# Kernel tuning notes

Measured on AMD Instinct MI355X. Metric: run time of the kernel, lower is better.

Reference implementation:

```python
import jax, jax.numpy as jnp
import numpy as np

B, C, H, W = 64, 192, 56, 56
NH, WS, SS = 6, 7, 3
HD = C // NH
N = WS * WS
MLP_H = int(C * 2.0)
EPS = 1e-5


def _layer_norm(x, g, b):
    m = jnp.mean(x, axis=-1, keepdims=True)
    v = jnp.mean(jnp.square(x - m), axis=-1, keepdims=True)
    return (x - m) * jax.lax.rsqrt(v + EPS) * g + b


def _window_partition(x):  # (B,H,W,C) -> (B*nW, N, C)
    b, h, w, c = x.shape
    x = x.reshape(b, h // WS, WS, w // WS, WS, c)
    return x.transpose(0, 1, 3, 2, 4, 5).reshape(-1, N, c)


def _window_reverse(win, h, w):  # (B*nW, N, C) -> (B,H,W,C)
    b = win.shape[0] // ((h // WS) * (w // WS))
    x = win.reshape(b, h // WS, w // WS, WS, WS, -1)
    return x.transpose(0, 1, 3, 2, 4, 5).reshape(b, h, w, -1)


def setup_inputs() -> dict:
    key = jax.random.key(0)
    ks = jax.random.split(key, 12)
    s = 0.02
    inp = {
        'query': jax.random.normal(ks[0], (B, C, H, W), jnp.float32),
        'norm_q_g': jnp.ones((C,), jnp.float32), 'norm_q_b': jnp.zeros((C,), jnp.float32),
        'norm_kv_g': jnp.ones((C,), jnp.float32), 'norm_kv_b': jnp.zeros((C,), jnp.float32),
        'Wq': jax.random.normal(ks[1], (C, C), jnp.float32) * s, 'bq': jnp.zeros((C,), jnp.float32),
        'Wk': jax.random.normal(ks[2], (C, C), jnp.float32) * s, 'bk': jnp.zeros((C,), jnp.float32),
        'Wv': jax.random.normal(ks[3], (C, C), jnp.float32) * s, 'bv': jnp.zeros((C,), jnp.float32),
        'rpb_table': jax.random.normal(ks[4], ((2 * WS - 1) ** 2, NH), jnp.float32) * s,
        'Wproj': jax.random.normal(ks[5], (C, C), jnp.float32) * s, 'bproj': jnp.zeros((C,), jnp.float32),
        'norm_ffn_g': jnp.ones((C,), jnp.float32), 'norm_ffn_b': jnp.zeros((C,), jnp.float32),
        'W1': jax.random.normal(ks[6], (C, MLP_H), jnp.float32) * s, 'b1': jnp.zeros((MLP_H,), jnp.float32),
        'W2': jax.random.normal(ks[7], (MLP_H, C), jnp.float32) * s, 'b2': jnp.zeros((C,), jnp.float32),
    }
    # relative position index (constant buffer)
    coords = np.stack(np.meshgrid(np.arange(WS), np.arange(WS), indexing='ij')).reshape(2, -1)
    rel = (coords[:, :, None] - coords[:, None, :]).transpose(1, 2, 0)
    rel[..., 0] += WS - 1
    rel[..., 1] += WS - 1
    rel[..., 0] *= 2 * WS - 1
    inp['rel_idx'] = jnp.asarray(rel.sum(-1), jnp.int32)  # (N, N)
    # shifted-window attention mask (constant buffer)
    img = np.zeros((H, W), np.float32)
    cnt = 0
    for hs in (slice(0, -WS), slice(-WS, -SS), slice(-SS, None)):
        for ws_ in (slice(0, -WS), slice(-WS, -SS), slice(-SS, None)):
            img[hs, ws_] = cnt
            cnt += 1
    mw = img.reshape(H // WS, WS, W // WS, WS).transpose(0, 2, 1, 3).reshape(-1, N)
    am = mw[:, None, :] - mw[:, :, None]  # (nW, N, N)
    inp['attn_mask'] = jnp.asarray(np.where(am != 0, -100.0, 0.0), np.float32)
    return inp


def reference(query, norm_q_g, norm_q_b, norm_kv_g, norm_kv_b, Wq, bq, Wk, bk, Wv, bv,
              rpb_table, Wproj, bproj, norm_ffn_g, norm_ffn_b, W1, b1, W2, b2,
              rel_idx, attn_mask):
    scale = HD ** (-0.5)
    x = query.reshape(B, C, H * W).transpose(0, 2, 1)  # (B, HW, C)
    shortcut = x
    qn = _layer_norm(x, norm_q_g, norm_q_b).reshape(B, H, W, C)
    kvn = _layer_norm(x, norm_kv_g, norm_kv_b).reshape(B, H, W, C)
    # cyclic shift
    qn = jnp.roll(qn, (-SS, -SS), axis=(1, 2))
    kvn = jnp.roll(kvn, (-SS, -SS), axis=(1, 2))
    q_win = _window_partition(qn)   # (B_, N, C)
    kv_win = _window_partition(kvn)
    B_ = q_win.shape[0]
    q = (q_win @ Wq + bq).reshape(B_, N, NH, HD).transpose(0, 2, 1, 3)
    k = (kv_win @ Wk + bk).reshape(B_, N, NH, HD).transpose(0, 2, 1, 3)
    v = (kv_win @ Wv + bv).reshape(B_, N, NH, HD).transpose(0, 2, 1, 3)
    attn = jnp.einsum('bhnd,bhmd->bhnm', q * scale, k)  # (B_, NH, N, N)
    bias = rpb_table[rel_idx.reshape(-1)].reshape(N, N, NH).transpose(2, 0, 1)
    attn = attn + bias[None]
    nW = attn_mask.shape[0]
    attn = attn.reshape(B_ // nW, nW, NH, N, N) + attn_mask[None, :, None]
    attn = attn.reshape(B_, NH, N, N)
    attn = jax.nn.softmax(attn, axis=-1)
    out = jnp.einsum('bhnm,bhmd->bhnd', attn, v).transpose(0, 2, 1, 3).reshape(B_, N, C)
    out = out @ Wproj + bproj
    x_sp = _window_reverse(out, H, W)
    x_sp = jnp.roll(x_sp, (SS, SS), axis=(1, 2))  # reverse shift
    x = shortcut + x_sp.reshape(B, H * W, C)
    h = _layer_norm(x, norm_ffn_g, norm_ffn_b)
    h = jax.nn.gelu(h @ W1 + b1, approximate=False) @ W2 + b2
    x = x + h
    return x.transpose(0, 2, 1).reshape(B, C, H, W)
```

## Files before the change

kernel.cpp:

```cpp
#include <hip/hip_runtime.h>
#include <hip/hip_bf16.h>
#include <math.h>

#define B_IMG 64
#define C_DIM 192
#define HW 3136
#define NTOK (B_IMG*HW)
#define NH 6
#define HD 32
#define WSZ 7
#define NTW 49
#define SS 3
#define NWIN 4096
#define NW64 262144
#define MLPH 384
#define EPS 1e-5f

typedef __attribute__((ext_vector_type(8))) short bfx8;
typedef __attribute__((ext_vector_type(4))) float f32x4;

__device__ __forceinline__ float u2f(unsigned short u){
    union { float f; unsigned int i; } v; v.i = ((unsigned int)u) << 16; return v.f;
}
__device__ __forceinline__ unsigned short f2u(float f){
    union { float f; unsigned int i; } v; v.f = f;
    unsigned int r = v.i + 0x7FFF + ((v.i >> 16) & 1);
    return (unsigned short)(r >> 16);
}
__device__ __forceinline__ unsigned int cvtpk(float lo, float hi){
    unsigned int r;
    asm("v_cvt_pk_bf16_f32 %0, %1, %2" : "=v"(r) : "v"(lo), "v"(hi));
    return r;
}
__device__ __forceinline__ void gl_lds16(const void* g, void* l){
    __builtin_amdgcn_global_load_lds(
        (const __attribute__((address_space(1))) unsigned int*)g,
        (__attribute__((address_space(3))) unsigned int*)l, 16, 0, 0);
}

__device__ __forceinline__ int rowmap(int w_, int n){
    int b  = w_ >> 6, wl = w_ & 63;
    int wy = wl >> 3, wx = wl & 7;
    int ty = n / 7,  tx = n % 7;
    int h = wy*7 + ty + SS; if (h >= 56) h -= 56;
    int w = wx*7 + tx + SS; if (w >= 56) w -= 56;
    return b*HW + h*56 + w;
}

__global__ void __launch_bounds__(256) p0_prep(
    const float* Wq, const float* bq, const float* Wk, const float* bk,
    const float* Wv, const float* bv, const float* Wproj,
    const float* W1, const float* b1, const float* W2,
    const float* gq, const float* nbq, const float* gkv, const float* nbkv,
    const float* gffn, const float* nbffn,
    const float* rpb, const int* rel_idx, const float* attn_mask,
    unsigned short* WqkvT, unsigned short* WprojT, unsigned short* W1T, unsigned short* W2T,
    float* bias_qkv, float* b1_e, unsigned short* comb,
    float* colsum_qkv, float* colsum1)
{
    const float scale = 0.17677669529663687f;
    int id = blockIdx.x*256 + threadIdx.x;
    if (id < 110592){
        int j = id/192, c = id - j*192;
        int which = j/192, col = j - which*192;
        float v;
        if (which==0)      v = scale*gq[c]*Wq[c*192+col];
        else if (which==1) v = gkv[c]*Wk[c*192+col];
        else               v = gkv[c]*Wv[c*192+col];
        WqkvT[id] = f2u(v);
    } else if (id < 147456){
        int t = id-110592; int co = t/192, k = t-co*192;
        WprojT[t] = f2u(Wproj[k*192+co]);
    } else if (id < 221184){
        int t = id-147456; int j = t/192, c = t-j*192;
        W1T[t] = f2u(gffn[c]*W1[c*384+j]);
    } else if (id < 294912){
        int t = id-221184; int co = t/384, k = t-co*384;
        W2T[t] = f2u(W2[k*192+co]);
    } else if (id < 295488){
        int j = id-294912; int which=j/192, col=j-which*192;
        float s;
        if (which==0){ s = bq[col]; for(int c=0;c<192;c++) s += nbq[c]*Wq[c*192+col]; s*=scale; }
        else if (which==1){ s = bk[col]; for(int c=0;c<192;c++) s += nbkv[c]*Wk[c*192+col]; }
        else { s = bv[col]; for(int c=0;c<192;c++) s += nbkv[c]*Wv[c*192+col]; }
        bias_qkv[j] = s;
    } else if (id < 295872){
        int j = id-295488; float s = b1[j];
        for(int c=0;c<192;c++) s += nbffn[c]*W1[c*384+j];
        b1_e[j] = s;
    } else if (id < 394176){
        int t = id-295872;
        int j = t & 63, i = (t>>6) & 63;
        int rest = t >> 12;
        int h = rest % 6, cls = rest / 6;
        float v = -1e30f;
        if (i < 49 && j < 49){
            int wlrep = (cls>>1)*56 + (cls&1)*7;
            v = rpb[rel_idx[i*49+j]*6 + h] + attn_mask[wlrep*2401 + i*49 + j];
        }
        comb[t] = f2u(v);
    } else if (id < 394752){
        int j = id-394176; int which=j/192, col=j-which*192;
        float s = 0.f;
        if (which==0){ for(int c=0;c<192;c++) s += gq[c]*Wq[c*192+col]; s*=scale; }
        else if (which==1){ for(int c=0;c<192;c++) s += gkv[c]*Wk[c*192+col]; }
        else { for(int c=0;c<192;c++) s += gkv[c]*Wv[c*192+col]; }
        colsum_qkv[j] = s;
    } else if (id < 395136){
        int j = id-394752; float s = 0.f;
        for(int c=0;c<192;c++) s += gffn[c]*W1[c*384+j];
        colsum1[j] = s;
    }
}

__global__ void __launch_bounds__(256) p1_transpose_stats(
    const float* q, unsigned short* X, float* mean, float* rstd)
{
    __shared__ float t[32*193];
    __shared__ float ms[32], rs[32];
    int blk = blockIdx.x;
    int b = blk / 98, tile = blk - b*98;
    int hw0 = tile*32;
    const float* qb = q + (size_t)b*C_DIM*HW;
    int hw_off = threadIdx.x & 31, csub = threadIdx.x >> 5;
    for (int cb = 0; cb < 192; cb += 8){
        int c = cb + csub;
        t[hw_off*193 + c] = qb[(size_t)c*HW + hw0 + hw_off];
    }
    __syncthreads();
    {
        int tt = threadIdx.x >> 3, qq = threadIdx.x & 7;
        float s=0.f, s2=0.f;
        #pragma unroll
        for (int i=0;i<24;i++){ float v = t[tt*193 + qq*24 + i]; s+=v; s2+=v*v; }
        s  += __shfl_xor(s,1);  s  += __shfl_xor(s,2);  s  += __shfl_xor(s,4);
        s2 += __shfl_xor(s2,1); s2 += __shfl_xor(s2,2); s2 += __shfl_xor(s2,4);
        if (qq==0){
            float m = s*(1.f/192.f);
            ms[tt] = m; rs[tt] = rsqrtf(s2*(1.f/192.f) - m*m + EPS);
        }
    }
    __syncthreads();
    int g0 = b*HW + hw0;
    if (threadIdx.x < 32){
        mean[g0+threadIdx.x] = ms[threadIdx.x];
        rstd[g0+threadIdx.x] = rs[threadIdx.x];
    }
    for (int i = threadIdx.x; i < 32*24; i += 256){
        int tt = i/24, cq = i - tt*24;
        int base = tt*193 + cq*8;
        int4 vr; unsigned int* pu = (unsigned int*)&vr;
        pu[0] = cvtpk(t[base+0], t[base+1]);
        pu[1] = cvtpk(t[base+2], t[base+3]);
        pu[2] = cvtpk(t[base+4], t[base+5]);
        pu[3] = cvtpk(t[base+6], t[base+7]);
        *(int4*)(X + (size_t)(g0+tt)*192 + cq*8) = vr;
    }
}

__global__ void __launch_bounds__(256) p2_qkv(
    const unsigned short* X, const float* mean, const float* rstd,
    const unsigned short* WqkvT, const float* bias_qkv, const float* colsum_qkv,
    unsigned short* Qb, unsigned short* Kb, unsigned short* Vt)
{
    __shared__ __align__(16) char L[32768];
    __shared__ int rowg[64];
    __shared__ __align__(16) float mr[64], rr[64];
    char* As = L; char* Bs = L + 8192;
    int which = blockIdx.y, bx = blockIdx.x;
    if (which < 2 && bx >= 3136) return;
    int t0 = bx*64;
    int tid = threadIdx.x, l = tid&63, wid = tid>>6;
    if (tid < 64){
        int w, n;
        if (which == 2){ w = bx; n = tid > 48 ? 48 : tid; }
        else { int t = t0 + tid; w = t/49; n = t - w*49; }
        int g = rowmap(w, n); rowg[tid]=g; mr[tid]=mean[g]; rr[tid]=rstd[g];
    }
    __syncthreads();
    f32x4 acc[4][3] = {};
    for (int kt=0; kt<3; ++kt){
        #pragma unroll
        for (int i=0;i<2;++i){
            int c = i*256 + tid;
            int row = c>>3, kq = (c&7) ^ (row&7);
            gl_lds16(X + (size_t)rowg[row]*192 + kt*64 + kq*8,
                     As + i*4096 + wid*1024);
        }
        #pragma unroll
        for (int i=0;i<6;++i){
            int c = i*256 + tid;
            int row = c>>3, kq = (c&7) ^ (row&7);
            gl_lds16(WqkvT + (size_t)(which*192+row)*192 + kt*64 + kq*8,
                     Bs + i*4096 + wid*1024);
        }
        __syncthreads();
        #pragma unroll
        for (int ks2=0; ks2<2; ++ks2){
            int kb = ks2*64 + ((l>>4)*16);
            bfx8 a[4], b[3];
            #pragma unroll
            for (int m=0;m<4;m++){ int r = m*16 + (l&15); a[m] = *(const bfx8*)(As + r*128 + (kb ^ ((r&7)<<4))); }
            #pragma unroll
            for (int n=0;n<3;n++){ int r = (wid*3+n)*16 + (l&15); b[n] = *(const bfx8*)(Bs + r*128 + (kb ^ ((r&7)<<4))); }
            #pragma unroll
            for (int m=0;m<4;m++)
                #pragma unroll
                for (int n=0;n<3;n++)
                    acc[m][n] = __builtin_amdgcn_mfma_f32_16x16x32_bf16(a[m], b[n], acc[m][n], 0,0,0);
        }
        __syncthreads();
    }
    unsigned short* Cs = (unsigned short*)L;
    #pragma unroll
    for (int m=0;m<4;m++){
        f32x4 m4 = *(const f32x4*)(mr + m*16 + (l>>4)*4);
        f32x4 r4 = *(const f32x4*)(rr + m*16 + (l>>4)*4);
        #pragma unroll
        for (int n=0;n<3;n++){
            int col = (wid*3+n)*16 + (l&15);
            float bv = bias_qkv[which*192 + col];
            float cs = colsum_qkv[which*192 + col];
            float v0 = r4[0]*(acc[m][n][0] - m4[0]*cs) + bv;
            float v1 = r4[1]*(acc[m][n][1] - m4[1]*cs) + bv;
            float v2 = r4[2]*(acc[m][n][2] - m4[2]*cs) + bv;
            float v3 = r4[3]*(acc[m][n][3] - m4[3]*cs) + bv;
            unsigned int p0 = cvtpk(v0,v1), p1 = cvtpk(v2,v3);
            int row = m*16 + (l>>4)*4;
            Cs[row*200 + col]     = (unsigned short)p0;
            Cs[(row+1)*200 + col] = (unsigned short)(p0>>16);
            Cs[(row+2)*200 + col] = (unsigned short)p1;
            Cs[(row+3)*200 + col] = (unsigned short)(p1>>16);
        }
    }
    __syncthreads();
    if (which < 2){
        unsigned short* dst = which==0 ? Qb : Kb;
        for (int c = tid; c < 64*24; c += 256){
            int row = c/24, cq = c-row*24;
            int4 v = *(const int4*)(Cs + row*200 + cq*8);
            *(int4*)(dst + (size_t)(t0+row)*192 + cq*8) = v;
        }
    } else {
        int w = bx;
        #pragma unroll
        for (int k=0;k<6;++k){
            int c = k*32 + (tid&31); int jo = tid>>5;
            int4 ov; unsigned short* os = (unsigned short*)&ov;
            #pragma unroll
            for (int e=0;e<8;++e) os[e] = Cs[(jo*8+e)*200 + c];
            *(int4*)(Vt + (size_t)c*NW64 + w*64 + jo*8) = ov;
        }
    }
}

__global__ void __launch_bounds__(128) p3_attn(
    const unsigned short* Qb, const unsigned short* Kb, const unsigned short* Vt,
    const unsigned short* comb, unsigned short* attn_h)
{
    __shared__ __align__(16) char PL[2][8448];
    int bid = blockIdx.x;
    int w = bid/3, yp = bid - w*3;
    int tid = threadIdx.x, l = tid & 63;
    int h = yp*2 + (tid>>6);
    char* P = PL[tid>>6];
    float* invr = (float*)(PL[tid>>6] + 8192);
    int q = l & 15, g = l >> 4;
    int wl = w & 63;
    int cls = (((wl>>3)==7) ? 2 : 0) + (((wl&7)==7) ? 1 : 0);

    bfx8 ak[4], bq[4];
    #pragma unroll
    for (int jt=0; jt<4; ++jt){
        int row = 16*jt + q; if (row > 48) row = 48;
        size_t base = (size_t)(w*49 + row)*192 + h*32 + g*8;
        ak[jt] = *(const bfx8*)(Kb + base);
        bq[jt] = *(const bfx8*)(Qb + base);
    }
    f32x4 s[4][4];
    {
        f32x4 z = {0.f,0.f,0.f,0.f};
        #pragma unroll
        for (int it=0; it<4; ++it)
            #pragma unroll
            for (int jt=0; jt<4; ++jt)
                s[it][jt] = __builtin_amdgcn_mfma_f32_16x16x32_bf16(ak[jt], bq[it], z, 0,0,0);
    }
    const unsigned short* cb = comb + ((size_t)(cls*6 + h) << 12);
    float sum[4];
    #pragma unroll
    for (int it=0; it<4; ++it){
        #pragma unroll
        for (int jt=0; jt<4; ++jt){
            uint2 c2 = *(const uint2*)(cb + (16*it + q)*64 + 16*jt + 4*g);
            const unsigned short* cs = (const unsigned short*)&c2;
            s[it][jt][0] += u2f(cs[0]);
            s[it][jt][1] += u2f(cs[1]);
            s[it][jt][2] += u2f(cs[2]);
            s[it][jt][3] += u2f(cs[3]);
        }
        float m = s[it][0][0];
        #pragma unroll
        for (int jt=0; jt<4; ++jt)
            #pragma unroll
            for (int r=0; r<4; ++r) m = fmaxf(m, s[it][jt][r]);
        m = fmaxf(m, __shfl_xor(m, 16));
        m = fmaxf(m, __shfl_xor(m, 32));
        float su = 0.f;
        #pragma unroll
        for (int jt=0; jt<4; ++jt)
            #pragma unroll
            for (int r=0; r<4; ++r){
                float e = __expf(s[it][jt][r] - m);
                s[it][jt][r] = e;
                su += e;
            }
        su += __shfl_xor(su, 16);
        su += __shfl_xor(su, 32);
        sum[it] = su;
    }
    #pragma unroll
    for (int it=0; it<4; ++it){
        int i = 16*it + q;
        #pragma unroll
        for (int jt=0; jt<4; ++jt){
            unsigned int w0 = cvtpk(s[it][jt][0], s[it][jt][1]);
            unsigned int w1 = cvtpk(s[it][jt][2], s[it][jt][3]);
            int jb = 32*jt + 8*g;
            *(uint2*)(P + i*128 + (jb ^ ((i&7)<<4))) = make_uint2(w0, w1);
        }
    }
    if (l < 16){
        #pragma unroll
        for (int it=0; it<4; ++it) invr[16*it + l] = 1.0f / sum[it];
    }
    __syncthreads();
    f32x4 o[4][2] = {};
    #pragma unroll
    for (int kt=0; kt<2; ++kt){
        bfx8 pa[4], vb[2];
        #pragma unroll
        for (int mt=0; mt<4; ++mt){
            int r = 16*mt + q;
            pa[mt] = *(const bfx8*)(P + r*128 + ((kt*64 + g*16) ^ ((r&7)<<4)));
        }
        #pragma unroll
        for (int nt=0; nt<2; ++nt){
            int d = 16*nt + q;
            vb[nt] = *(const bfx8*)(Vt + (size_t)(h*32 + d)*NW64 + w*64 + kt*32 + g*8);
        }
        #pragma unroll
        for (int mt=0; mt<4; ++mt)
            #pragma unroll
            for (int nt=0; nt<2; ++nt)
                o[mt][nt] = __builtin_amdgcn_mfma_f32_16x16x32_bf16(pa[mt], vb[nt], o[mt][nt], 0,0,0);
    }
    #pragma unroll
    for (int mt=0; mt<4; ++mt){
        f32x4 iv = *(const f32x4*)(invr + 16*mt + 4*g);
        #pragma unroll
        for (int nt=0; nt<2; ++nt){
            int d = 16*nt + q;
            #pragma unroll
            for (int r=0; r<4; ++r){
                int i = 16*mt + 4*g + r;
                if (i < 49)
                    attn_h[((size_t)h*NTOK + (size_t)w*49 + i)*32 + d] = f2u(o[mt][nt][r] * iv[r]);
            }
        }
    }
}

__global__ void __launch_bounds__(256) p4_proj(
    const unsigned short* attn_h, const unsigned short* WprojT, const float* bproj,
    const unsigned short* X, unsigned short* x2, float* mean2, float* rstd2)
{
    __shared__ __align__(16) char L[32768];
    __shared__ int rowg[64];
    char* As = L; char* Bs = L + 8192;
    int t0 = blockIdx.x*64;
    int tid = threadIdx.x, l = tid&63, wid = tid>>6;
    if (tid < 64){
        int t = t0 + tid; int w = t/49, n = t - w*49;
        rowg[tid] = rowmap(w, n);
    }
    __syncthreads();
    f32x4 acc[4][3] = {};
    for (int kt=0; kt<3; ++kt){
        #pragma unroll
        for (int i=0;i<2;++i){
            int c = i*256 + tid;
            int row = c>>3, kq = (c&7) ^ (row&7);
            int hh = kt*2 + (kq>>2), kin = kq&3;
            gl_lds16(attn_h + ((size_t)hh*NTOK + t0+row)*32 + kin*8,
                     As + i*4096 + wid*1024);
        }
        #pragma unroll
        for (int i=0;i<6;++i){
            int c = i*256 + tid;
            int row = c>>3, kq = (c&7) ^ (row&7);
            gl_lds16(WprojT + (size_t)row*192 + kt*64 + kq*8,
                     Bs + i*4096 + wid*1024);
        }
        __syncthreads();
        #pragma unroll
        for (int ks2=0; ks2<2; ++ks2){
            int kb = ks2*64 + ((l>>4)*16);
            bfx8 a[4], b[3];
            #pragma unroll
            for (int m=0;m<4;m++){ int r = m*16 + (l&15); a[m] = *(const bfx8*)(As + r*128 + (kb ^ ((r&7)<<4))); }
            #pragma unroll
            for (int n=0;n<3;n++){ int r = (wid*3+n)*16 + (l&15); b[n] = *(const bfx8*)(Bs + r*128 + (kb ^ ((r&7)<<4))); }
            #pragma unroll
            for (int m=0;m<4;m++)
                #pragma unroll
                for (int n=0;n<3;n++)
                    acc[m][n] = __builtin_amdgcn_mfma_f32_16x16x32_bf16(a[m], b[n], acc[m][n], 0,0,0);
        }
        __syncthreads();
    }
    unsigned short* bounce = (unsigned short*)L;
    #pragma unroll
    for (int m=0;m<4;m++)
        #pragma unroll
        for (int n=0;n<3;n++){
            int col = (wid*3+n)*16 + (l&15);
            float bv = bproj[col];
            #pragma unroll
            for (int r=0;r<4;r++){
                int row = m*16 + (l>>4)*4 + r;
                int g = rowg[row];
                bounce[row*200 + col] = f2u(acc[m][n][r] + bv + u2f(X[(size_t)g*192 + col]));
            }
        }
    __syncthreads();
    {
        int row = tid>>2, q = tid&3;
        float s=0.f, s2=0.f;
        #pragma unroll
        for (int i=0;i<6;i++){
            int4 v = *(const int4*)(bounce + row*200 + q*48 + i*8);
            const unsigned short* vs=(const unsigned short*)&v;
            #pragma unroll
            for(int e=0;e<8;e++){ float f=u2f(vs[e]); s+=f; s2+=f*f; }
        }
        s  += __shfl_xor(s,1);  s  += __shfl_xor(s,2);
        s2 += __shfl_xor(s2,1); s2 += __shfl_xor(s2,2);
        if (q==0){
            float m = s*(1.f/192.f);
            mean2[rowg[row]] = m;
            rstd2[rowg[row]] = rsqrtf(s2*(1.f/192.f) - m*m + EPS);
        }
    }
    for (int c = tid; c < 64*24; c += 256){
        int row = c/24, cq = c-row*24;
        int4 v = *(const int4*)(bounce + row*200 + cq*8);
        *(int4*)(x2 + (size_t)rowg[row]*192 + cq*8) = v;
    }
}

__global__ void __launch_bounds__(256) p5_mlp1(
    const unsigned short* x2, const float* mean2, const float* rstd2,
    const unsigned short* W1T, const float* b1_e, const float* colsum1,
    unsigned short* hidden)
{
    __shared__ __align__(16) char L[32768];
    __shared__ __align__(16) float mr[64], rr[64];
    char* As = L; char* Bs = L + 8192;
    int t0 = blockIdx.x*64; int nh = blockIdx.y;
    int tid = threadIdx.x, l = tid&63, wid = tid>>6;
    if (tid < 64){ mr[tid]=mean2[t0+tid]; rr[tid]=rstd2[t0+tid]; }
    __syncthreads();
    f32x4 acc[4][3] = {};
    for (int kt=0; kt<3; ++kt){
        #pragma unroll
        for (int i=0;i<2;++i){
            int c = i*256 + tid;
            int row = c>>3, kq = (c&7) ^ (row&7);
            gl_lds16(x2 + (size_t)(t0+row)*192 + kt*64 + kq*8,
                     As + i*4096 + wid*1024);
        }
        #pragma unroll
        for (int i=0;i<6;++i){
            int c = i*256 + tid;
            int row = c>>3, kq = (c&7) ^ (row&7);
            gl_lds16(W1T + (size_t)(nh*192+row)*192 + kt*64 + kq*8,
                     Bs + i*4096 + wid*1024);
        }
        __syncthreads();
        #pragma unroll
        for (int ks2=0; ks2<2; ++ks2){
            int kb = ks2*64 + ((l>>4)*16);
            bfx8 a[4], b[3];
            #pragma unroll
            for (int m=0;m<4;m++){ int r = m*16 + (l&15); a[m] = *(const bfx8*)(As + r*128 + (kb ^ ((r&7)<<4))); }
            #pragma unroll
            for (int n=0;n<3;n++){ int r = (wid*3+n)*16 + (l&15); b[n] = *(const bfx8*)(Bs + r*128 + (kb ^ ((r&7)<<4))); }
            #pragma unroll
            for (int m=0;m<4;m++)
                #pragma unroll
                for (int n=0;n<3;n++)
                    acc[m][n] = __builtin_amdgcn_mfma_f32_16x16x32_bf16(a[m], b[n], acc[m][n], 0,0,0);
        }
        __syncthreads();
    }
    unsigned short* bounce = (unsigned short*)L;
    #pragma unroll
    for (int m=0;m<4;m++){
        f32x4 m4 = *(const f32x4*)(mr + m*16 + (l>>4)*4);
        f32x4 r4 = *(const f32x4*)(rr + m*16 + (l>>4)*4);
        #pragma unroll
        for (int n=0;n<3;n++){
            int col = (wid*3+n)*16 + (l&15);
            float bv = b1_e[nh*192 + col];
            float cs = colsum1[nh*192 + col];
            float gv[4];
            #pragma unroll
            for (int r=0;r<4;r++){
                float v = r4[r]*(acc[m][n][r] - m4[r]*cs) + bv;
                gv[r] = 0.5f*v*(1.0f + erff(v*0.70710678118654752f));
            }
            unsigned int p0 = cvtpk(gv[0],gv[1]), p1 = cvtpk(gv[2],gv[3]);
            int row = m*16 + (l>>4)*4;
            bounce[row*200 + col]     = (unsigned short)p0;
            bounce[(row+1)*200 + col] = (unsigned short)(p0>>16);
            bounce[(row+2)*200 + col] = (unsigned short)p1;
            bounce[(row+3)*200 + col] = (unsigned short)(p1>>16);
        }
    }
    __syncthreads();
    for (int c = tid; c < 64*24; c += 256){
        int row = c/24, cq = c-row*24;
        int4 v = *(const int4*)(bounce + row*200 + cq*8);
        *(int4*)(hidden + (size_t)(t0+row)*384 + nh*192 + cq*8) = v;
    }
}

__global__ void __launch_bounds__(256) p6_mlp2(
    const unsigned short* hidden, const unsigned short* W2T, const float* b2,
    const unsigned short* x2, float* out)
{
    __shared__ __align__(16) char L[32768];
    char* As = L; char* Bs = L + 8192;
    int t0 = blockIdx.x*64;
    int tid = threadIdx.x, l = tid&63, wid = tid>>6;
    f32x4 acc[4][3] = {};
    for (int kt=0; kt<6; ++kt){
        #pragma unroll
        for (int i=0;i<2;++i){
            int c = i*256 + tid;
            int row = c>>3, kq = (c&7) ^ (row&7);
            gl_lds16(hidden + (size_t)(t0+row)*384 + kt*64 + kq*8,
                     As + i*4096 + wid*1024);
        }
        #pragma unroll
        for (int i=0;i<6;++i){
            int c = i*256 + tid;
            int row = c>>3, kq = (c&7) ^ (row&7);
            gl_lds16(W2T + (size_t)row*384 + kt*64 + kq*8,
                     Bs + i*4096 + wid*1024);
        }
        __syncthreads();
        #pragma unroll
        for (int ks2=0; ks2<2; ++ks2){
            int kb = ks2*64 + ((l>>4)*16);
            bfx8 a[4], b[3];
            #pragma unroll
            for (int m=0;m<4;m++){ int r = m*16 + (l&15); a[m] = *(const bfx8*)(As + r*128 + (kb ^ ((r&7)<<4))); }
            #pragma unroll
            for (int n=0;n<3;n++){ int r = (wid*3+n)*16 + (l&15); b[n] = *(const bfx8*)(Bs + r*128 + (kb ^ ((r&7)<<4))); }
            #pragma unroll
            for (int m=0;m<4;m++)
                #pragma unroll
                for (int n=0;n<3;n++)
                    acc[m][n] = __builtin_amdgcn_mfma_f32_16x16x32_bf16(a[m], b[n], acc[m][n], 0,0,0);
        }
        __syncthreads();
    }
    float* bounce = (float*)L;
    int bimg = t0 / HW, hw0 = t0 - bimg*HW;
    #pragma unroll
    for (int half=0; half<2; ++half){
        #pragma unroll
        for (int mm=0;mm<2;mm++){
            int m = half*2 + mm;
            #pragma unroll
            for (int n=0;n<3;n++){
                int col = (wid*3+n)*16 + (l&15);
                float bv = b2[col];
                #pragma unroll
                for (int r=0;r<4;r++){
                    int row = m*16 + (l>>4)*4 + r;
                    bounce[(row - half*32)*197 + col] = acc[m][n][r] + bv + u2f(x2[(size_t)(t0+row)*192 + col]);
                }
            }
        }
        __syncthreads();
        int hw0h = hw0 + half*32;
        for (int i = tid; i < 32*192; i += 256){
            int cc = i>>5, hwoff = i&31;
            out[(size_t)(bimg*192 + cc)*HW + hw0h + hwoff] = bounce[hwoff*197 + cc];
        }
        __syncthreads();
    }
}

extern "C" void kernel_launch(void* const* d_in, const int* in_sizes, int n_in,
                              void* d_out, int out_size, void* d_ws, size_t ws_size,
                              hipStream_t stream) {
    const float* query = (const float*)d_in[0];
    const float* gq    = (const float*)d_in[1];
    const float* nbq   = (const float*)d_in[2];
    const float* gkv   = (const float*)d_in[3];
    const float* nbkv  = (const float*)d_in[4];
    const float* Wq    = (const float*)d_in[5];
    const float* bq    = (const float*)d_in[6];
    const float* Wk    = (const float*)d_in[7];
    const float* bk    = (const float*)d_in[8];
    const float* Wv    = (const float*)d_in[9];
    const float* bv    = (const float*)d_in[10];
    const float* rpb   = (const float*)d_in[11];
    const float* Wproj = (const float*)d_in[12];
    const float* bproj = (const float*)d_in[13];
    const float* gffn  = (const float*)d_in[14];
    const float* nbffn = (const float*)d_in[15];
    const float* W1    = (const float*)d_in[16];
    const float* b1    = (const float*)d_in[17];
    const float* W2    = (const float*)d_in[18];
    const float* b2    = (const float*)d_in[19];
    const int*   rel_idx   = (const int*)d_in[20];
    const float* attn_mask = (const float*)d_in[21];
    float* out = (float*)d_out;

    char* wsb = (char*)d_ws;
    size_t off = 0;
    auto alloc = [&](size_t bytes)->void*{
        void* p = wsb + off; off += (bytes + 255) & ~(size_t)255; return p;
    };
    unsigned short* X      = (unsigned short*)alloc((size_t)NTOK*192*2);
    unsigned short* Qb     = (unsigned short*)alloc((size_t)NTOK*192*2);
    unsigned short* Kb     = (unsigned short*)alloc((size_t)NTOK*192*2);
    unsigned short* Vt     = (unsigned short*)alloc((size_t)192*NW64*2);
    unsigned short* attn_h = (unsigned short*)alloc((size_t)NH*NTOK*32*2);
    float* mean  = (float*)alloc((size_t)NTOK*4);
    float* rstd  = (float*)alloc((size_t)NTOK*4);
    unsigned short* WqkvT = (unsigned short*)alloc(110592*2);
    unsigned short* WprojT= (unsigned short*)alloc(36864*2);
    unsigned short* W1T   = (unsigned short*)alloc(73728*2);
    unsigned short* W2T   = (unsigned short*)alloc(73728*2);
    float* bias_qkv = (float*)alloc(576*4);
    float* b1_e     = (float*)alloc(384*4);
    unsigned short* comb = (unsigned short*)alloc((size_t)4*6*64*64*2);
    float* colsum_qkv = (float*)alloc(576*4);
    float* colsum1    = (float*)alloc(384*4);
    unsigned short* hidden = Qb;
    unsigned short* x2     = Vt;
    float* mean2 = mean;
    float* rstd2 = rstd;

    hipLaunchKernelGGL(p0_prep, dim3(1544), dim3(256), 0, stream,
        Wq, bq, Wk, bk, Wv, bv, Wproj, W1, b1, W2,
        gq, nbq, gkv, nbkv, gffn, nbffn, rpb, rel_idx, attn_mask,
        WqkvT, WprojT, W1T, W2T, bias_qkv, b1_e, comb, colsum_qkv, colsum1);
    hipLaunchKernelGGL(p1_transpose_stats, dim3(64*98), dim3(256), 0, stream,
        query, X, mean, rstd);
    hipLaunchKernelGGL(p2_qkv, dim3(NWIN, 3), dim3(256), 0, stream,
        X, mean, rstd, WqkvT, bias_qkv, colsum_qkv, Qb, Kb, Vt);
    hipLaunchKernelGGL(p3_attn, dim3(NWIN*3), dim3(128), 0, stream,
        Qb, Kb, Vt, comb, attn_h);
    hipLaunchKernelGGL(p4_proj, dim3(NTOK/64), dim3(256), 0, stream,
        attn_h, WprojT, bproj, X, x2, mean2, rstd2);
    hipLaunchKernelGGL(p5_mlp1, dim3(NTOK/64, 2), dim3(256), 0, stream,
        x2, mean2, rstd2, W1T, b1_e, colsum1, hidden);
    hipLaunchKernelGGL(p6_mlp2, dim3(NTOK/64), dim3(256), 0, stream,
        hidden, W2T, b2, x2, out);
}
```

Before: 477.6 us.

## Prefetch next K tile into LDS while MFMAs run on register-held fragments

In the QKV, projection, MLP1 and MLP2 GEMM kernels, each iteration now reads the whole current K tile from LDS into registers, then issues the global-to-LDS loads for the next tile before running the MFMAs. This overlaps global memory latency with matrix math inside a single LDS buffer, without adding double buffering. It costs extra VGPRs for the held fragments and changes the barrier placement, which could lower occupancy.

```diff
diff --git a/kernel.cpp b/kernel.cpp
--- a/kernel.cpp
+++ b/kernel.cpp
@@ -178,38 +178,49 @@
         int g = rowmap(w, n); rowg[tid]=g; mr[tid]=mean[g]; rr[tid]=rstd[g];
     }
     __syncthreads();
+    #pragma unroll
+    for (int i=0;i<2;++i){
+        int c = i*256 + tid; int row = c>>3, kq = (c&7) ^ (row&7);
+        gl_lds16(X + (size_t)rowg[row]*192 + kq*8, As + i*4096 + wid*1024);
+    }
+    #pragma unroll
+    for (int i=0;i<6;++i){
+        int c = i*256 + tid; int row = c>>3, kq = (c&7) ^ (row&7);
+        gl_lds16(WqkvT + (size_t)(which*192+row)*192 + kq*8, Bs + i*4096 + wid*1024);
+    }
+    __syncthreads();
     f32x4 acc[4][3] = {};
+    bfx8 a[2][4], b[2][3];
     for (int kt=0; kt<3; ++kt){
-        #pragma unroll
-        for (int i=0;i<2;++i){
-            int c = i*256 + tid;
-            int row = c>>3, kq = (c&7) ^ (row&7);
-            gl_lds16(X + (size_t)rowg[row]*192 + kt*64 + kq*8,
-                     As + i*4096 + wid*1024);
-        }
-        #pragma unroll
-        for (int i=0;i<6;++i){
-            int c = i*256 + tid;
-            int row = c>>3, kq = (c&7) ^ (row&7);
-            gl_lds16(WqkvT + (size_t)(which*192+row)*192 + kt*64 + kq*8,
-                     Bs + i*4096 + wid*1024);
-        }
-        __syncthreads();
         #pragma unroll
         for (int ks2=0; ks2<2; ++ks2){
             int kb = ks2*64 + ((l>>4)*16);
-            bfx8 a[4], b[3];
-            #pragma unroll
-            for (int m=0;m<4;m++){ int r = m*16 + (l&15); a[m] = *(const bfx8*)(As + r*128 + (kb ^ ((r&7)<<4))); }
-            #pragma unroll
-            for (int n=0;n<3;n++){ int r = (wid*3+n)*16 + (l&15); b[n] = *(const bfx8*)(Bs + r*128 + (kb ^ ((r&7)<<4))); }
+            #pragma unroll
+            for (int m=0;m<4;m++){ int r = m*16 + (l&15); a[ks2][m] = *(const bfx8*)(As + r*128 + (kb ^ ((r&7)<<4))); }
+            #pragma unroll
+            for (int n=0;n<3;n++){ int r = (wid*3+n)*16 + (l&15); b[ks2][n] = *(const bfx8*)(Bs + r*128 + (kb ^ ((r&7)<<4))); }
+        }
+        __syncthreads();
+        if (kt < 2){
+            #pragma unroll
+            for (int i=0;i<2;++i){
+                int c = i*256 + tid; int row = c>>3, kq = (c&7) ^ (row&7);
+                gl_lds16(X + (size_t)rowg[row]*192 + (kt+1)*64 + kq*8, As + i*4096 + wid*1024);
+            }
+            #pragma unroll
+            for (int i=0;i<6;++i){
+                int c = i*256 + tid; int row = c>>3, kq = (c&7) ^ (row&7);
+                gl_lds16(WqkvT + (size_t)(which*192+row)*192 + (kt+1)*64 + kq*8, Bs + i*4096 + wid*1024);
+            }
+        }
+        #pragma unroll
+        for (int ks2=0; ks2<2; ++ks2)
             #pragma unroll
             for (int m=0;m<4;m++)
                 #pragma unroll
                 for (int n=0;n<3;n++)
-                    acc[m][n] = __builtin_amdgcn_mfma_f32_16x16x32_bf16(a[m], b[n], acc[m][n], 0,0,0);
-        }
-        __syncthreads();
+                    acc[m][n] = __builtin_amdgcn_mfma_f32_16x16x32_bf16(a[ks2][m], b[ks2][n], acc[m][n], 0,0,0);
+        if (kt < 2) __syncthreads();
     }
     unsigned short* Cs = (unsigned short*)L;
     #pragma unroll
@@ -385,39 +396,51 @@
         rowg[tid] = rowmap(w, n);
     }
     __syncthreads();
+    #pragma unroll
+    for (int i=0;i<2;++i){
+        int c = i*256 + tid; int row = c>>3, kq = (c&7) ^ (row&7);
+        int hh = kq>>2, kin = kq&3;
+        gl_lds16(attn_h + ((size_t)hh*NTOK + t0+row)*32 + kin*8, As + i*4096 + wid*1024);
+    }
+    #pragma unroll
+    for (int i=0;i<6;++i){
+        int c = i*256 + tid; int row = c>>3, kq = (c&7) ^ (row&7);
+        gl_lds16(WprojT + (size_t)row*192 + kq*8, Bs + i*4096 + wid*1024);
+    }
+    __syncthreads();
     f32x4 acc[4][3] = {};
+    bfx8 a[2][4], b[2][3];
     for (int kt=0; kt<3; ++kt){
-        #pragma unroll
-        for (int i=0;i<2;++i){
-            int c = i*256 + tid;
-            int row = c>>3, kq = (c&7) ^ (row&7);
-            int hh = kt*2 + (kq>>2), kin = kq&3;
-            gl_lds16(attn_h + ((size_t)hh*NTOK + t0+row)*32 + kin*8,
-                     As + i*4096 + wid*1024);
-        }
-        #pragma unroll
-        for (int i=0;i<6;++i){
-            int c = i*256 + tid;
-            int row = c>>3, kq = (c&7) ^ (row&7);
-            gl_lds16(WprojT + (size_t)row*192 + kt*64 + kq*8,
-                     Bs + i*4096 + wid*1024);
-        }
-        __syncthreads();
         #pragma unroll
         for (int ks2=0; ks2<2; ++ks2){
             int kb = ks2*64 + ((l>>4)*16);
-            bfx8 a[4], b[3];
-            #pragma unroll
-            for (int m=0;m<4;m++){ int r = m*16 + (l&15); a[m] = *(const bfx8*)(As + r*128 + (kb ^ ((r&7)<<4))); }
-            #pragma unroll
-            for (int n=0;n<3;n++){ int r = (wid*3+n)*16 + (l&15); b[n] = *(const bfx8*)(Bs + r*128 + (kb ^ ((r&7)<<4))); }
+            #pragma unroll
+            for (int m=0;m<4;m++){ int r = m*16 + (l&15); a[ks2][m] = *(const bfx8*)(As + r*128 + (kb ^ ((r&7)<<4))); }
+            #pragma unroll
+            for (int n=0;n<3;n++){ int r = (wid*3+n)*16 + (l&15); b[ks2][n] = *(const bfx8*)(Bs + r*128 + (kb ^ ((r&7)<<4))); }
+        }
+        __syncthreads();
+        if (kt < 2){
+            #pragma unroll
+            for (int i=0;i<2;++i){
+                int c = i*256 + tid; int row = c>>3, kq = (c&7) ^ (row&7);
+                int hh = (kt+1)*2 + (kq>>2), kin = kq&3;
+                gl_lds16(attn_h + ((size_t)hh*NTOK + t0+row)*32 + kin*8, As + i*4096 + wid*1024);
+            }
+            #pragma unroll
+            for (int i=0;i<6;++i){
+                int c = i*256 + tid; int row = c>>3, kq = (c&7) ^ (row&7);
+                gl_lds16(WprojT + (size_t)row*192 + (kt+1)*64 + kq*8, Bs + i*4096 + wid*1024);
+            }
+        }
+        #pragma unroll
+        for (int ks2=0; ks2<2; ++ks2)
             #pragma unroll
             for (int m=0;m<4;m++)
                 #pragma unroll
                 for (int n=0;n<3;n++)
-                    acc[m][n] = __builtin_amdgcn_mfma_f32_16x16x32_bf16(a[m], b[n], acc[m][n], 0,0,0);
-        }
-        __syncthreads();
+                    acc[m][n] = __builtin_amdgcn_mfma_f32_16x16x32_bf16(a[ks2][m], b[ks2][n], acc[m][n], 0,0,0);
+        if (kt < 2) __syncthreads();
     }
     unsigned short* bounce = (unsigned short*)L;
     #pragma unroll
@@ -470,39 +493,49 @@
     int t0 = blockIdx.x*64; int nh = blockIdx.y;
     int tid = threadIdx.x, l = tid&63, wid = tid>>6;
     if (tid < 64){ mr[tid]=mean2[t0+tid]; rr[tid]=rstd2[t0+tid]; }
+    #pragma unroll
+    for (int i=0;i<2;++i){
+        int c = i*256 + tid; int row = c>>3, kq = (c&7) ^ (row&7);
+        gl_lds16(x2 + (size_t)(t0+row)*192 + kq*8, As + i*4096 + wid*1024);
+    }
+    #pragma unroll
+    for (int i=0;i<6;++i){
+        int c = i*256 + tid; int row = c>>3, kq = (c&7) ^ (row&7);
+        gl_lds16(W1T + (size_t)(nh*192+row)*192 + kq*8, Bs + i*4096 + wid*1024);
+    }
     __syncthreads();
     f32x4 acc[4][3] = {};
+    bfx8 a[2][4], b[2][3];
     for (int kt=0; kt<3; ++kt){
-        #pragma unroll
-        for (int i=0;i<2;++i){
-            int c = i*256 + tid;
-            int row = c>>3, kq = (c&7) ^ (row&7);
-            gl_lds16(x2 + (size_t)(t0+row)*192 + kt*64 + kq*8,
-                     As + i*4096 + wid*1024);
-        }
-        #pragma unroll
-        for (int i=0;i<6;++i){
-            int c = i*256 + tid;
-            int row = c>>3, kq = (c&7) ^ (row&7);
-            gl_lds16(W1T + (size_t)(nh*192+row)*192 + kt*64 + kq*8,
-                     Bs + i*4096 + wid*1024);
-        }
-        __syncthreads();
         #pragma unroll
         for (int ks2=0; ks2<2; ++ks2){
             int kb = ks2*64 + ((l>>4)*16);
-            bfx8 a[4], b[3];
-            #pragma unroll
-            for (int m=0;m<4;m++){ int r = m*16 + (l&15); a[m] = *(const bfx8*)(As + r*128 + (kb ^ ((r&7)<<4))); }
-            #pragma unroll
-            for (int n=0;n<3;n++){ int r = (wid*3+n)*16 + (l&15); b[n] = *(const bfx8*)(Bs + r*128 + (kb ^ ((r&7)<<4))); }
+            #pragma unroll
+            for (int m=0;m<4;m++){ int r = m*16 + (l&15); a[ks2][m] = *(const bfx8*)(As + r*128 + (kb ^ ((r&7)<<4))); }
+            #pragma unroll
+            for (int n=0;n<3;n++){ int r = (wid*3+n)*16 + (l&15); b[ks2][n] = *(const bfx8*)(Bs + r*128 + (kb ^ ((r&7)<<4))); }
+        }
+        __syncthreads();
+        if (kt < 2){
+            #pragma unroll
+            for (int i=0;i<2;++i){
+                int c = i*256 + tid; int row = c>>3, kq = (c&7) ^ (row&7);
+                gl_lds16(x2 + (size_t)(t0+row)*192 + (kt+1)*64 + kq*8, As + i*4096 + wid*1024);
+            }
+            #pragma unroll
+            for (int i=0;i<6;++i){
+                int c = i*256 + tid; int row = c>>3, kq = (c&7) ^ (row&7);
+                gl_lds16(W1T + (size_t)(nh*192+row)*192 + (kt+1)*64 + kq*8, Bs + i*4096 + wid*1024);
+            }
+        }
+        #pragma unroll
+        for (int ks2=0; ks2<2; ++ks2)
             #pragma unroll
             for (int m=0;m<4;m++)
                 #pragma unroll
                 for (int n=0;n<3;n++)
-                    acc[m][n] = __builtin_amdgcn_mfma_f32_16x16x32_bf16(a[m], b[n], acc[m][n], 0,0,0);
-        }
-        __syncthreads();
+                    acc[m][n] = __builtin_amdgcn_mfma_f32_16x16x32_bf16(a[ks2][m], b[ks2][n], acc[m][n], 0,0,0);
+        if (kt < 2) __syncthreads();
     }
     unsigned short* bounce = (unsigned short*)L;
     #pragma unroll
@@ -544,38 +577,49 @@
     char* As = L; char* Bs = L + 8192;
     int t0 = blockIdx.x*64;
     int tid = threadIdx.x, l = tid&63, wid = tid>>6;
+    #pragma unroll
+    for (int i=0;i<2;++i){
+        int c = i*256 + tid; int row = c>>3, kq = (c&7) ^ (row&7);
+        gl_lds16(hidden + (size_t)(t0+row)*384 + kq*8, As + i*4096 + wid*1024);
+    }
+    #pragma unroll
+    for (int i=0;i<6;++i){
+        int c = i*256 + tid; int row = c>>3, kq = (c&7) ^ (row&7);
+        gl_lds16(W2T + (size_t)row*384 + kq*8, Bs + i*4096 + wid*1024);
+    }
+    __syncthreads();
     f32x4 acc[4][3] = {};
+    bfx8 a[2][4], b[2][3];
     for (int kt=0; kt<6; ++kt){
-        #pragma unroll
-        for (int i=0;i<2;++i){
-            int c = i*256 + tid;
-            int row = c>>3, kq = (c&7) ^ (row&7);
-            gl_lds16(hidden + (size_t)(t0+row)*384 + kt*64 + kq*8,
-                     As + i*4096 + wid*1024);
-        }
-        #pragma unroll
-        for (int i=0;i<6;++i){
-            int c = i*256 + tid;
-            int row = c>>3, kq = (c&7) ^ (row&7);
-            gl_lds16(W2T + (size_t)row*384 + kt*64 + kq*8,
-                     Bs + i*4096 + wid*1024);
-        }
-        __syncthreads();
         #pragma unroll
         for (int ks2=0; ks2<2; ++ks2){
             int kb = ks2*64 + ((l>>4)*16);
-            bfx8 a[4], b[3];
-            #pragma unroll
-            for (int m=0;m<4;m++){ int r = m*16 + (l&15); a[m] = *(const bfx8*)(As + r*128 + (kb ^ ((r&7)<<4))); }
-            #pragma unroll
-            for (int n=0;n<3;n++){ int r = (wid*3+n)*16 + (l&15); b[n] = *(const bfx8*)(Bs + r*128 + (kb ^ ((r&7)<<4))); }
+            #pragma unroll
+            for (int m=0;m<4;m++){ int r = m*16 + (l&15); a[ks2][m] = *(const bfx8*)(As + r*128 + (kb ^ ((r&7)<<4))); }
+            #pragma unroll
+            for (int n=0;n<3;n++){ int r = (wid*3+n)*16 + (l&15); b[ks2][n] = *(const bfx8*)(Bs + r*128 + (kb ^ ((r&7)<<4))); }
+        }
+        __syncthreads();
+        if (kt < 5){
+            #pragma unroll
+            for (int i=0;i<2;++i){
+                int c = i*256 + tid; int row = c>>3, kq = (c&7) ^ (row&7);
+                gl_lds16(hidden + (size_t)(t0+row)*384 + (kt+1)*64 + kq*8, As + i*4096 + wid*1024);
+            }
+            #pragma unroll
+            for (int i=0;i<6;++i){
+                int c = i*256 + tid; int row = c>>3, kq = (c&7) ^ (row&7);
+                gl_lds16(W2T + (size_t)row*384 + (kt+1)*64 + kq*8, Bs + i*4096 + wid*1024);
+            }
+        }
+        #pragma unroll
+        for (int ks2=0; ks2<2; ++ks2)
             #pragma unroll
             for (int m=0;m<4;m++)
                 #pragma unroll
                 for (int n=0;n<3;n++)
-                    acc[m][n] = __builtin_amdgcn_mfma_f32_16x16x32_bf16(a[m], b[n], acc[m][n], 0,0,0);
-        }
-        __syncthreads();
+                    acc[m][n] = __builtin_amdgcn_mfma_f32_16x16x32_bf16(a[ks2][m], b[ks2][n], acc[m][n], 0,0,0);
+        if (kt < 5) __syncthreads();
     }
     float* bounce = (float*)L;
     int bimg = t0 / HW, hw0 = t0 - bimg*HW;
```

New measurement: 489.0 us. 2.4% more time.

## Fuse MLP fc1 and fc2 kernels, keeping hidden activations in LDS

Applied to the files above, without the earlier changes.

Merges the two MLP GEMM kernels into one kernel per 64-token tile. The kernel computes fc1+GELU for each 192-wide half of the hidden dimension into a padded LDS buffer, then accumulates the fc2 contribution from that half directly. This removes the global write and re-read of the bf16 hidden tensor and one kernel launch. In exchange LDS per block grows to about 52KB, which may lower occupancy. The x2 tile is also reloaded for the second half, and the loads are not double-buffered.

```diff
diff --git a/kernel.cpp b/kernel.cpp
--- a/kernel.cpp
+++ b/kernel.cpp
@@ -15,6 +15,7 @@
 #define NW64 262144
 #define MLPH 384
 #define EPS 1e-5f
+#define HS 216
 
 typedef __attribute__((ext_vector_type(8))) short bfx8;
 typedef __attribute__((ext_vector_type(4))) float f32x4;
@@ -459,131 +460,115 @@
     }
 }
 
-__global__ void __launch_bounds__(256) p5_mlp1(
+__global__ void __launch_bounds__(256) p56_mlp(
     const unsigned short* x2, const float* mean2, const float* rstd2,
     const unsigned short* W1T, const float* b1_e, const float* colsum1,
-    unsigned short* hidden)
+    const unsigned short* W2T, const float* b2, float* out)
 {
-    __shared__ __align__(16) char L[32768];
+    __shared__ __align__(16) char L[27648 + 24576];
     __shared__ __align__(16) float mr[64], rr[64];
-    char* As = L; char* Bs = L + 8192;
-    int t0 = blockIdx.x*64; int nh = blockIdx.y;
+    char* R0 = L;
+    char* Bs = L + 27648;
+    int t0 = blockIdx.x*64;
     int tid = threadIdx.x, l = tid&63, wid = tid>>6;
     if (tid < 64){ mr[tid]=mean2[t0+tid]; rr[tid]=rstd2[t0+tid]; }
     __syncthreads();
-    f32x4 acc[4][3] = {};
-    for (int kt=0; kt<3; ++kt){
-        #pragma unroll
-        for (int i=0;i<2;++i){
-            int c = i*256 + tid;
-            int row = c>>3, kq = (c&7) ^ (row&7);
-            gl_lds16(x2 + (size_t)(t0+row)*192 + kt*64 + kq*8,
-                     As + i*4096 + wid*1024);
-        }
-        #pragma unroll
-        for (int i=0;i<6;++i){
-            int c = i*256 + tid;
-            int row = c>>3, kq = (c&7) ^ (row&7);
-            gl_lds16(W1T + (size_t)(nh*192+row)*192 + kt*64 + kq*8,
-                     Bs + i*4096 + wid*1024);
+    f32x4 oacc[4][3] = {};
+    for (int half=0; half<2; ++half){
+        f32x4 acc[4][3] = {};
+        for (int kt=0; kt<3; ++kt){
+            #pragma unroll
+            for (int i=0;i<2;++i){
+                int c = i*256 + tid;
+                int row = c>>3, kq = (c&7) ^ (row&7);
+                gl_lds16(x2 + (size_t)(t0+row)*192 + kt*64 + kq*8,
+                         R0 + i*4096 + wid*1024);
+            }
+            #pragma unroll
+            for (int i=0;i<6;++i){
+                int c = i*256 + tid;
+                int row = c>>3, kq = (c&7) ^ (row&7);
+                gl_lds16(W1T + (size_t)(half*192+row)*192 + kt*64 + kq*8,
+                         Bs + i*4096 + wid*1024);
+            }
+            __syncthreads();
+            #pragma unroll
+            for (int ks2=0; ks2<2; ++ks2){
+                int kb = ks2*64 + ((l>>4)*16);
+                bfx8 a[4], b[3];
+                #pragma unroll
+                for (int m=0;m<4;m++){ int r = m*16 + (l&15); a[m] = *(const bfx8*)(R0 + r*128 + (kb ^ ((r&7)<<4))); }
+                #pragma unroll
+                for (int n=0;n<3;n++){ int r = (wid*3+n)*16 + (l&15); b[n] = *(const bfx8*)(Bs + r*128 + (kb ^ ((r&7)<<4))); }
+                #pragma unroll
+                for (int m=0;m<4;m++)
+                    #pragma unroll
+                    for (int n=0;n<3;n++)
+                        acc[m][n] = __builtin_amdgcn_mfma_f32_16x16x32_bf16(a[m], b[n], acc[m][n], 0,0,0);
+            }
+            __syncthreads();
+        }
+        unsigned short* H = (unsigned short*)R0;
+        #pragma unroll
+        for (int m=0;m<4;m++){
+            f32x4 m4 = *(const f32x4*)(mr + m*16 + (l>>4)*4);
+            f32x4 r4 = *(const f32x4*)(rr + m*16 + (l>>4)*4);
+            #pragma unroll
+            for (int n=0;n<3;n++){
+                int col = (wid*3+n)*16 + (l&15);
+                float bv = b1_e[half*192 + col];
+                float cs = colsum1[half*192 + col];
+                float gv[4];
+                #pragma unroll
+                for (int r=0;r<4;r++){
+                    float v = r4[r]*(acc[m][n][r] - m4[r]*cs) + bv;
+                    gv[r] = 0.5f*v*(1.0f + erff(v*0.70710678118654752f));
+                }
+                unsigned int p0 = cvtpk(gv[0],gv[1]), p1 = cvtpk(gv[2],gv[3]);
+                int row = m*16 + (l>>4)*4;
+                H[row*HS + col]     = (unsigned short)p0;
+                H[(row+1)*HS + col] = (unsigned short)(p0>>16);
+                H[(row+2)*HS + col] = (unsigned short)p1;
+                H[(row+3)*HS + col] = (unsigned short)(p1>>16);
+            }
         }
         __syncthreads();
-        #pragma unroll
-        for (int ks2=0; ks2<2; ++ks2){
-            int kb = ks2*64 + ((l>>4)*16);
-            bfx8 a[4], b[3];
-            #pragma unroll
-            for (int m=0;m<4;m++){ int r = m*16 + (l&15); a[m] = *(const bfx8*)(As + r*128 + (kb ^ ((r&7)<<4))); }
-            #pragma unroll
-            for (int n=0;n<3;n++){ int r = (wid*3+n)*16 + (l&15); b[n] = *(const bfx8*)(Bs + r*128 + (kb ^ ((r&7)<<4))); }
-            #pragma unroll
-            for (int m=0;m<4;m++)
-                #pragma unroll
-                for (int n=0;n<3;n++)
-                    acc[m][n] = __builtin_amdgcn_mfma_f32_16x16x32_bf16(a[m], b[n], acc[m][n], 0,0,0);
-        }
-        __syncthreads();
-    }
-    unsigned short* bounce = (unsigned short*)L;
-    #pragma unroll
-    for (int m=0;m<4;m++){
-        f32x4 m4 = *(const f32x4*)(mr + m*16 + (l>>4)*4);
-        f32x4 r4 = *(const f32x4*)(rr + m*16 + (l>>4)*4);
-        #pragma unroll
-        for (int n=0;n<3;n++){
-            int col = (wid*3+n)*16 + (l&15);
-            float bv = b1_e[nh*192 + col];
-            float cs = colsum1[nh*192 + col];
-            float gv[4];
-            #pragma unroll
-            for (int r=0;r<4;r++){
-                float v = r4[r]*(acc[m][n][r] - m4[r]*cs) + bv;
-                gv[r] = 0.5f*v*(1.0f + erff(v*0.70710678118654752f));
-            }
-            unsigned int p0 = cvtpk(gv[0],gv[1]), p1 = cvtpk(gv[2],gv[3]);
-            int row = m*16 + (l>>4)*4;
-            bounce[row*200 + col]     = (unsigned short)p0;
-            bounce[(row+1)*200 + col] = (unsigned short)(p0>>16);
-            bounce[(row+2)*200 + col] = (unsigned short)p1;
-            bounce[(row+3)*200 + col] = (unsigned short)(p1>>16);
-        }
-    }
-    __syncthreads();
-    for (int c = tid; c < 64*24; c += 256){
-        int row = c/24, cq = c-row*24;
-        int4 v = *(const int4*)(bounce + row*200 + cq*8);
-        *(int4*)(hidden + (size_t)(t0+row)*384 + nh*192 + cq*8) = v;
-    }
-}
-
-__global__ void __launch_bounds__(256) p6_mlp2(
-    const unsigned short* hidden, const unsigned short* W2T, const float* b2,
-    const unsigned short* x2, float* out)
-{
-    __shared__ __align__(16) char L[32768];
-    char* As = L; char* Bs = L + 8192;
-    int t0 = blockIdx.x*64;
-    int tid = threadIdx.x, l = tid&63, wid = tid>>6;
-    f32x4 acc[4][3] = {};
-    for (int kt=0; kt<6; ++kt){
-        #pragma unroll
-        for (int i=0;i<2;++i){
-            int c = i*256 + tid;
-            int row = c>>3, kq = (c&7) ^ (row&7);
-            gl_lds16(hidden + (size_t)(t0+row)*384 + kt*64 + kq*8,
-                     As + i*4096 + wid*1024);
-        }
-        #pragma unroll
-        for (int i=0;i<6;++i){
-            int c = i*256 + tid;
-            int row = c>>3, kq = (c&7) ^ (row&7);
-            gl_lds16(W2T + (size_t)row*384 + kt*64 + kq*8,
-                     Bs + i*4096 + wid*1024);
-        }
-        __syncthreads();
-        #pragma unroll
-        for (int ks2=0; ks2<2; ++ks2){
-            int kb = ks2*64 + ((l>>4)*16);
-            bfx8 a[4], b[3];
-            #pragma unroll
-            for (int m=0;m<4;m++){ int r = m*16 + (l&15); a[m] = *(const bfx8*)(As + r*128 + (kb ^ ((r&7)<<4))); }
-            #pragma unroll
-            for (int n=0;n<3;n++){ int r = (wid*3+n)*16 + (l&15); b[n] = *(const bfx8*)(Bs + r*128 + (kb ^ ((r&7)<<4))); }
-            #pragma unroll
-            for (int m=0;m<4;m++)
-                #pragma unroll
-                for (int n=0;n<3;n++)
-                    acc[m][n] = __builtin_amdgcn_mfma_f32_16x16x32_bf16(a[m], b[n], acc[m][n], 0,0,0);
-        }
-        __syncthreads();
-    }
-    float* bounce = (float*)L;
+        for (int kt2=0; kt2<3; ++kt2){
+            #pragma unroll
+            for (int i=0;i<6;++i){
+                int c = i*256 + tid;
+                int row = c>>3, kq = (c&7) ^ (row&7);
+                gl_lds16(W2T + (size_t)row*384 + half*192 + kt2*64 + kq*8,
+                         Bs + i*4096 + wid*1024);
+            }
+            __syncthreads();
+            #pragma unroll
+            for (int ks2=0; ks2<2; ++ks2){
+                int kbB = ks2*64 + ((l>>4)*16);
+                bfx8 a[4], b[3];
+                #pragma unroll
+                for (int m=0;m<4;m++){
+                    int r = m*16 + (l&15);
+                    a[m] = *(const bfx8*)(H + r*HS + kt2*64 + ks2*32 + (l>>4)*8);
+                }
+                #pragma unroll
+                for (int n=0;n<3;n++){ int r = (wid*3+n)*16 + (l&15); b[n] = *(const bfx8*)(Bs + r*128 + (kbB ^ ((r&7)<<4))); }
+                #pragma unroll
+                for (int m=0;m<4;m++)
+                    #pragma unroll
+                    for (int n=0;n<3;n++)
+                        oacc[m][n] = __builtin_amdgcn_mfma_f32_16x16x32_bf16(a[m], b[n], oacc[m][n], 0,0,0);
+            }
+            __syncthreads();
+        }
+    }
+    float* bounce = (float*)R0;
     int bimg = t0 / HW, hw0 = t0 - bimg*HW;
     #pragma unroll
-    for (int half=0; half<2; ++half){
+    for (int hf=0; hf<2; ++hf){
         #pragma unroll
         for (int mm=0;mm<2;mm++){
-            int m = half*2 + mm;
+            int m = hf*2 + mm;
             #pragma unroll
             for (int n=0;n<3;n++){
                 int col = (wid*3+n)*16 + (l&15);
@@ -591,12 +576,12 @@
                 #pragma unroll
                 for (int r=0;r<4;r++){
                     int row = m*16 + (l>>4)*4 + r;
-                    bounce[(row - half*32)*197 + col] = acc[m][n][r] + bv + u2f(x2[(size_t)(t0+row)*192 + col]);
+                    bounce[(row - hf*32)*197 + col] = oacc[m][n][r] + bv + u2f(x2[(size_t)(t0+row)*192 + col]);
                 }
             }
         }
         __syncthreads();
-        int hw0h = hw0 + half*32;
+        int hw0h = hw0 + hf*32;
         for (int i = tid; i < 32*192; i += 256){
             int cc = i>>5, hwoff = i&31;
             out[(size_t)(bimg*192 + cc)*HW + hw0h + hwoff] = bounce[hwoff*197 + cc];
@@ -653,7 +638,6 @@
     unsigned short* comb = (unsigned short*)alloc((size_t)4*6*64*64*2);
     float* colsum_qkv = (float*)alloc(576*4);
     float* colsum1    = (float*)alloc(384*4);
-    unsigned short* hidden = Qb;
     unsigned short* x2     = Vt;
     float* mean2 = mean;
     float* rstd2 = rstd;
@@ -670,8 +654,6 @@
         Qb, Kb, Vt, comb, attn_h);
     hipLaunchKernelGGL(p4_proj, dim3(NTOK/64), dim3(256), 0, stream,
         attn_h, WprojT, bproj, X, x2, mean2, rstd2);
-    hipLaunchKernelGGL(p5_mlp1, dim3(NTOK/64, 2), dim3(256), 0, stream,
-        x2, mean2, rstd2, W1T, b1_e, colsum1, hidden);
-    hipLaunchKernelGGL(p6_mlp2, dim3(NTOK/64), dim3(256), 0, stream,
-        hidden, W2T, b2, x2, out);
-}
+    hipLaunchKernelGGL(p56_mlp, dim3(NTOK/64), dim3(256), 0, stream,
+        x2, mean2, rstd2, W1T, b1_e, colsum1, W2T, b2, out);
+}
```

Measured after the change: 466.4 us (median of 2 runs). -2.3%, faster.
